# Performance work log

Measured on AMD Instinct MI355X. Metric: run time of the kernel, lower is better.

Reference implementation:

```python
import jax, jax.numpy as jnp
import numpy as np

# Grid configuration (from PointBasedTransformConfig / data dict)
G = 64                      # mast3r grid size per axis
NUM_VOXELS = G * G * G      # 262144
K = 16                      # max_points_in_voxel
RES = 0.02                  # mast3r_grid_resolution
MIN_CORNER = -(G * RES) / 2.0  # cube centered at origin, side G*RES = 1.28
N_POINTS = 2_000_000


def setup_inputs() -> dict:
    key = jax.random.key(0)
    k1, k2, k3, k4 = jax.random.split(key, 4)
    # points uniform in [-0.8, 0.8]^3 so roughly half are inside the 1.28 cube
    pts_0 = (jax.random.uniform(k1, (N_POINTS, 3), dtype=jnp.float32) - 0.5) * 1.6
    conf = jax.random.uniform(k2, (N_POINTS,), dtype=jnp.float32)
    desc = jax.random.normal(k3, (N_POINTS, 24), dtype=jnp.float32)
    desc_conf = jax.random.normal(k4, (N_POINTS,), dtype=jnp.float32)
    return {"pts_0": pts_0, "conf": conf, "desc": desc, "desc_conf": desc_conf}


def _voxelize(pts_0, conf):
    """Returns pts_in_grid: (NUM_VOXELS, K) int32 point indices (or -1)."""
    n = pts_0.shape[0]
    # voxel index per point; out-of-bounds points get sentinel id NUM_VOXELS
    idx = jnp.floor((pts_0 - MIN_CORNER) / RES).astype(jnp.int32)  # (N,3)
    valid = jnp.all((idx >= 0) & (idx < G), axis=-1)               # (N,)
    vox = idx[:, 0] * (G * G) + idx[:, 1] * G + idx[:, 2]
    vox = jnp.where(valid, vox, NUM_VOXELS)
    # stable sort by confidence, descending (jnp.argsort is stable)
    order_conf = jnp.argsort(-conf)                 # point ids, conf-desc order
    vox_c = vox[order_conf]
    # stable sort by voxel id (preserves conf-desc order within each voxel)
    order_vox = jnp.argsort(vox_c)
    vox_s = vox_c[order_vox]                        # sorted voxel ids
    pid_s = order_conf[order_vox]                   # original point ids
    # bincount + exclusive cumsum -> per-voxel offsets -> position within voxel
    counts = jnp.bincount(vox_s, length=NUM_VOXELS + 1)
    offsets = jnp.cumsum(counts) - counts
    pos = jnp.arange(n, dtype=jnp.int32) - offsets[vox_s].astype(jnp.int32)
    # capacity-bounded scatter of point ids into the voxel grid
    ok = (pos < K) & (vox_s < NUM_VOXELS)
    rows = jnp.where(ok, vox_s, NUM_VOXELS)         # dump row for rejects
    cols = jnp.where(ok, pos, 0)
    vals = jnp.where(ok, pid_s, -1).astype(jnp.int32)
    grid = jnp.full((NUM_VOXELS + 1, K), -1, dtype=jnp.int32)
    grid = grid.at[rows, cols].set(vals)
    return grid[:NUM_VOXELS]


def reference(pts_0, conf, desc, desc_conf):
    pts_in_grid = _voxelize(pts_0, conf)            # (V, K) int32
    # gather per-point features into the grid; empty slots -> 0
    feat = jnp.concatenate(
        [pts_0, conf[:, None], desc, desc_conf[:, None]], axis=-1
    )                                               # (N, 29)
    safe = jnp.maximum(pts_in_grid, 0)
    occ = (pts_in_grid >= 0)[..., None].astype(feat.dtype)
    X = feat[safe] * occ                            # (V, K, 29)
    return pts_in_grid, X
```

## Files before the change

kernel.cpp:

```cpp
#include <hip/hip_runtime.h>
#include <limits.h>
#include <math.h>

#define GRID 64
#define NUM_VOXELS (GRID * GRID * GRID)
#define KSLOTS 16
#define CAP 32
#define FEAT 29

typedef float f32x4 __attribute__((ext_vector_type(4)));

__global__ __launch_bounds__(256) void scatter_kernel(
    const float* __restrict__ pts, const float* __restrict__ conf, int n,
    int* __restrict__ cnt, unsigned long long* __restrict__ buf) {
    int i = blockIdx.x * blockDim.x + threadIdx.x;
    if (i >= n) return;
    const float minc = (float)(-(64.0 * 0.02) / 2.0);
    const float rinv = 50.0f;
    float x = pts[(size_t)i * 3 + 0];
    float y = pts[(size_t)i * 3 + 1];
    float z = pts[(size_t)i * 3 + 2];
    int ix = (int)floorf((x - minc) * rinv);
    int iy = (int)floorf((y - minc) * rinv);
    int iz = (int)floorf((z - minc) * rinv);
    if ((unsigned)ix >= GRID || (unsigned)iy >= GRID || (unsigned)iz >= GRID) return;
    int v = ix * (GRID * GRID) + iy * GRID + iz;
    int pos = atomicAdd(&cnt[v], 1);
    if (pos < CAP) {
        unsigned int cb = __float_as_uint(conf[i]);
        unsigned long long key =
            ((unsigned long long)cb << 32) | (unsigned int)(~i);
        buf[(size_t)v * CAP + pos] = key;
    }
}

__global__ __launch_bounds__(256) void select_kernel(
    const int* __restrict__ cnt, const unsigned long long* __restrict__ buf,
    float* __restrict__ out_idx, float* __restrict__ stagedC) {
    int v = blockIdx.x * blockDim.x + threadIdx.x;
    if (v >= NUM_VOXELS) return;
    unsigned long long top[KSLOTS];
    #pragma unroll
    for (int s = 0; s < KSLOTS; ++s) top[s] = 0ULL;
    int n = cnt[v];
    if (n > CAP) n = CAP;
    const unsigned long long* row = buf + (size_t)v * CAP;
    for (int j = 0; j < n; ++j) {
        unsigned long long key = row[j];
        #pragma unroll
        for (int s = 0; s < KSLOTS; ++s) {
            unsigned long long hi = key > top[s] ? key : top[s];
            unsigned long long lo = key > top[s] ? top[s] : key;
            top[s] = hi;
            key    = lo;
        }
    }
    float* o = out_idx + (size_t)v * KSLOTS;
    float* c = stagedC + (size_t)v * KSLOTS;
    #pragma unroll
    for (int s = 0; s < KSLOTS; ++s) {
        unsigned long long k = top[s];
        o[s] = (float)((k != 0ULL) ? (int)(~(unsigned int)k) : -1);
        c[s] = __uint_as_float((unsigned int)(k >> 32));
    }
}

__global__ __launch_bounds__(256) void gather_kernel(
    const float* __restrict__ pts, const float* __restrict__ stagedC,
    const float* __restrict__ desc, const float* __restrict__ desc_conf,
    const float* __restrict__ out_idx, float* __restrict__ out_feat) {
    const int t = threadIdx.x;
    const size_t slot0 = (size_t)blockIdx.x * 256;
    const size_t slot  = slot0 + t;
    __shared__ __align__(16) float st[256 * FEAT];
    int pid = (int)out_idx[slot];
    float f[FEAT];
    #pragma unroll
    for (int e = 0; e < FEAT; ++e) f[e] = 0.0f;
    if (pid >= 0) {
        f[0] = pts[(size_t)pid * 3 + 0];
        f[1] = pts[(size_t)pid * 3 + 1];
        f[2] = pts[(size_t)pid * 3 + 2];
        f[3] = stagedC[slot];
        const f32x4* d4 = (const f32x4*)(desc) + (size_t)pid * 6;
        #pragma unroll
        for (int q = 0; q < 6; ++q) {
            f32x4 d = d4[q];
            f[4 + q * 4 + 0] = d.x; f[4 + q * 4 + 1] = d.y;
            f[4 + q * 4 + 2] = d.z; f[4 + q * 4 + 3] = d.w;
        }
        f[28] = desc_conf[pid];
    }
    #pragma unroll
    for (int e = 0; e < FEAT; ++e) st[t * FEAT + e] = f[e];
    __syncthreads();
    f32x4* dst = (f32x4*)(out_feat + slot0 * FEAT);
    const f32x4* src = (const f32x4*)st;
    #pragma unroll
    for (int k = t; k < 256 * FEAT / 4; k += 256)
        __builtin_nontemporal_store(src[k], &dst[k]);
}

__global__ __launch_bounds__(256) void select_kernel_nf(
    const int* __restrict__ cnt, const unsigned long long* __restrict__ buf,
    float* __restrict__ out_idx) {
    int v = blockIdx.x * blockDim.x + threadIdx.x;
    if (v >= NUM_VOXELS) return;
    unsigned long long top[KSLOTS];
    #pragma unroll
    for (int s = 0; s < KSLOTS; ++s) top[s] = 0ULL;
    int n = cnt[v];
    if (n > CAP) n = CAP;
    const unsigned long long* row = buf + (size_t)v * CAP;
    for (int j = 0; j < n; ++j) {
        unsigned long long key = row[j];
        #pragma unroll
        for (int s = 0; s < KSLOTS; ++s) {
            unsigned long long hi = key > top[s] ? key : top[s];
            unsigned long long lo = key > top[s] ? top[s] : key;
            top[s] = hi;
            key    = lo;
        }
    }
    float* o = out_idx + (size_t)v * KSLOTS;
    #pragma unroll
    for (int s = 0; s < KSLOTS; ++s) {
        unsigned long long k = top[s];
        o[s] = (float)((k != 0ULL) ? (int)(~(unsigned int)k) : -1);
    }
}

__global__ __launch_bounds__(256) void gather_kernel_nf(
    const float* __restrict__ pts, const float* __restrict__ conf,
    const float* __restrict__ desc, const float* __restrict__ desc_conf,
    const float* __restrict__ out_idx, float* __restrict__ out_feat) {
    const int t = threadIdx.x;
    const size_t slot0 = (size_t)blockIdx.x * 256;
    const size_t slot  = slot0 + t;
    __shared__ __align__(16) float st[256 * FEAT];
    int pid = (int)out_idx[slot];
    float f[FEAT];
    #pragma unroll
    for (int e = 0; e < FEAT; ++e) f[e] = 0.0f;
    if (pid >= 0) {
        f[0] = pts[(size_t)pid * 3 + 0];
        f[1] = pts[(size_t)pid * 3 + 1];
        f[2] = pts[(size_t)pid * 3 + 2];
        f[3] = conf[pid];
        const f32x4* d4 = (const f32x4*)(desc) + (size_t)pid * 6;
        #pragma unroll
        for (int q = 0; q < 6; ++q) {
            f32x4 d = d4[q];
            f[4 + q * 4 + 0] = d.x; f[4 + q * 4 + 1] = d.y;
            f[4 + q * 4 + 2] = d.z; f[4 + q * 4 + 3] = d.w;
        }
        f[28] = desc_conf[pid];
    }
    #pragma unroll
    for (int e = 0; e < FEAT; ++e) st[t * FEAT + e] = f[e];
    __syncthreads();
    f32x4* dst = (f32x4*)(out_feat + slot0 * FEAT);
    const f32x4* src = (const f32x4*)st;
    #pragma unroll
    for (int k = t; k < 256 * FEAT / 4; k += 256)
        __builtin_nontemporal_store(src[k], &dst[k]);
}

extern "C" void kernel_launch(void* const* d_in, const int* in_sizes, int n_in,
                              void* d_out, int out_size, void* d_ws, size_t ws_size,
                              hipStream_t stream) {
    const float* pts       = (const float*)d_in[0];
    const float* conf      = (const float*)d_in[1];
    const float* desc      = (const float*)d_in[2];
    const float* desc_conf = (const float*)d_in[3];
    const int n = in_sizes[1];

    float* out_idx  = (float*)d_out;
    float* out_feat = out_idx + (size_t)NUM_VOXELS * KSLOTS;

    const size_t sz_cnt  = (size_t)NUM_VOXELS * 4;
    const size_t sz_buf  = (size_t)NUM_VOXELS * CAP * 8;
    const size_t sz_stgc = (size_t)NUM_VOXELS * KSLOTS * 4;

    if (ws_size >= sz_cnt + sz_buf + sz_stgc) {
        int* cnt = (int*)d_ws;
        unsigned long long* buf = (unsigned long long*)((char*)d_ws + sz_cnt);
        float* stagedC = (float*)((char*)d_ws + sz_cnt + sz_buf);
        (void)hipMemsetAsync(cnt, 0, sz_cnt, stream);
        scatter_kernel<<<(n + 255) / 256, 256, 0, stream>>>(pts, conf, n, cnt, buf);
        select_kernel<<<NUM_VOXELS / 256, 256, 0, stream>>>(cnt, buf, out_idx, stagedC);
        gather_kernel<<<(NUM_VOXELS * KSLOTS) / 256, 256, 0, stream>>>(
            pts, stagedC, desc, desc_conf, out_idx, out_feat);
    } else {
        int* cnt = (int*)out_feat;
        unsigned long long* buf = (unsigned long long*)(out_feat + NUM_VOXELS);
        (void)hipMemsetAsync(cnt, 0, sz_cnt, stream);
        scatter_kernel<<<(n + 255) / 256, 256, 0, stream>>>(pts, conf, n, cnt, buf);
        select_kernel_nf<<<NUM_VOXELS / 256, 256, 0, stream>>>(cnt, buf, out_idx);
        gather_kernel_nf<<<(NUM_VOXELS * KSLOTS) / 256, 256, 0, stream>>>(
            pts, conf, desc, desc_conf, out_idx, out_feat);
    }
}
```

Baseline: 226.7 us.

## Carry point coords and desc_conf in voxel buffer to cut random gathers

The scatter kernel now writes a 32-byte record per point: a sort key (conf bits, a 21-bit point id, room for the slot index) plus x, y, z and desc_conf. The select kernel recovers the payload through the slot index in the winning key and stages coordinates, conf and desc_conf contiguously per output slot. The gather kernel then only randomly fetches desc, which removes scattered pts and desc_conf reads. In exchange the scatter buffer grows fourfold (256 MB of workspace), scatter and select write more, and the fast path now requires n to fit in 21 bits.

```diff
diff --git a/kernel.cpp b/kernel.cpp
--- a/kernel.cpp
+++ b/kernel.cpp
@@ -7,12 +7,15 @@
 #define KSLOTS 16
 #define CAP 32
 #define FEAT 29
+#define PIDBITS 0x1FFFFFu
 
 typedef float f32x4 __attribute__((ext_vector_type(4)));
+typedef unsigned long long u64;
 
 __global__ __launch_bounds__(256) void scatter_kernel(
-    const float* __restrict__ pts, const float* __restrict__ conf, int n,
-    int* __restrict__ cnt, unsigned long long* __restrict__ buf) {
+    const float* __restrict__ pts, const float* __restrict__ conf,
+    const float* __restrict__ desc_conf, int n,
+    int* __restrict__ cnt, u64* __restrict__ buf) {
     int i = blockIdx.x * blockDim.x + threadIdx.x;
     if (i >= n) return;
     const float minc = (float)(-(64.0 * 0.02) / 2.0);
@@ -28,60 +31,76 @@
     int pos = atomicAdd(&cnt[v], 1);
     if (pos < CAP) {
         unsigned int cb = __float_as_uint(conf[i]);
-        unsigned long long key =
-            ((unsigned long long)cb << 32) | (unsigned int)(~i);
-        buf[(size_t)v * CAP + pos] = key;
+        unsigned int lo = ((~(unsigned)i) & PIDBITS) << 11;
+        u64* e = buf + ((size_t)v * CAP + pos) * 4;
+        e[0] = ((u64)cb << 32) | lo;
+        f32x4 pl = {x, y, z, desc_conf[i]};
+        *(f32x4*)(e + 2) = pl;
     }
 }
 
 __global__ __launch_bounds__(256) void select_kernel(
-    const int* __restrict__ cnt, const unsigned long long* __restrict__ buf,
-    float* __restrict__ out_idx, float* __restrict__ stagedC) {
+    const int* __restrict__ cnt, const u64* __restrict__ buf,
+    float* __restrict__ out_idx, f32x4* __restrict__ stagedA,
+    float* __restrict__ stagedB) {
     int v = blockIdx.x * blockDim.x + threadIdx.x;
     if (v >= NUM_VOXELS) return;
-    unsigned long long top[KSLOTS];
+    u64 top[KSLOTS];
     #pragma unroll
     for (int s = 0; s < KSLOTS; ++s) top[s] = 0ULL;
     int n = cnt[v];
     if (n > CAP) n = CAP;
-    const unsigned long long* row = buf + (size_t)v * CAP;
+    const u64* row = buf + (size_t)v * CAP * 4;
     for (int j = 0; j < n; ++j) {
-        unsigned long long key = row[j];
+        u64 key = row[(size_t)j * 4] | (unsigned)j;
         #pragma unroll
         for (int s = 0; s < KSLOTS; ++s) {
-            unsigned long long hi = key > top[s] ? key : top[s];
-            unsigned long long lo = key > top[s] ? top[s] : key;
+            u64 hi = key > top[s] ? key : top[s];
+            u64 lo = key > top[s] ? top[s] : key;
             top[s] = hi;
             key    = lo;
         }
     }
-    float* o = out_idx + (size_t)v * KSLOTS;
-    float* c = stagedC + (size_t)v * KSLOTS;
+    float* o  = out_idx + (size_t)v * KSLOTS;
+    f32x4* sa = stagedA + (size_t)v * KSLOTS;
+    float* sb = stagedB + (size_t)v * KSLOTS;
     #pragma unroll
     for (int s = 0; s < KSLOTS; ++s) {
-        unsigned long long k = top[s];
-        o[s] = (float)((k != 0ULL) ? (int)(~(unsigned int)k) : -1);
-        c[s] = __uint_as_float((unsigned int)(k >> 32));
+        u64 a = top[s];
+        float pidf = -1.0f;
+        f32x4 pl = {0.0f, 0.0f, 0.0f, 0.0f};
+        float dc = 0.0f;
+        if (a != 0ULL) {
+            int j = (int)(a & 31u);
+            f32x4 p = *(const f32x4*)(row + (size_t)j * 4 + 2);
+            int pid = (int)(PIDBITS & ~(unsigned)(a >> 11));
+            pidf = (float)pid;
+            pl.x = p.x; pl.y = p.y; pl.z = p.z;
+            pl.w = __uint_as_float((unsigned)(a >> 32));
+            dc = p.w;
+        }
+        o[s]  = pidf;
+        sa[s] = pl;
+        sb[s] = dc;
     }
 }
 
 __global__ __launch_bounds__(256) void gather_kernel(
-    const float* __restrict__ pts, const float* __restrict__ stagedC,
-    const float* __restrict__ desc, const float* __restrict__ desc_conf,
+    const f32x4* __restrict__ stagedA, const float* __restrict__ stagedB,
+    const float* __restrict__ desc,
     const float* __restrict__ out_idx, float* __restrict__ out_feat) {
     const int t = threadIdx.x;
     const size_t slot0 = (size_t)blockIdx.x * 256;
     const size_t slot  = slot0 + t;
     __shared__ __align__(16) float st[256 * FEAT];
     int pid = (int)out_idx[slot];
+    f32x4 a = stagedA[slot];
+    float dc = stagedB[slot];
     float f[FEAT];
     #pragma unroll
     for (int e = 0; e < FEAT; ++e) f[e] = 0.0f;
+    f[0] = a.x; f[1] = a.y; f[2] = a.z; f[3] = a.w; f[28] = dc;
     if (pid >= 0) {
-        f[0] = pts[(size_t)pid * 3 + 0];
-        f[1] = pts[(size_t)pid * 3 + 1];
-        f[2] = pts[(size_t)pid * 3 + 2];
-        f[3] = stagedC[slot];
         const f32x4* d4 = (const f32x4*)(desc) + (size_t)pid * 6;
         #pragma unroll
         for (int q = 0; q < 6; ++q) {
@@ -89,7 +108,6 @@
             f[4 + q * 4 + 0] = d.x; f[4 + q * 4 + 1] = d.y;
             f[4 + q * 4 + 2] = d.z; f[4 + q * 4 + 3] = d.w;
         }
-        f[28] = desc_conf[pid];
     }
     #pragma unroll
     for (int e = 0; e < FEAT; ++e) st[t * FEAT + e] = f[e];
@@ -101,23 +119,45 @@
         __builtin_nontemporal_store(src[k], &dst[k]);
 }
 
+__global__ __launch_bounds__(256) void scatter_kernel_nf(
+    const float* __restrict__ pts, const float* __restrict__ conf, int n,
+    int* __restrict__ cnt, u64* __restrict__ buf) {
+    int i = blockIdx.x * blockDim.x + threadIdx.x;
+    if (i >= n) return;
+    const float minc = (float)(-(64.0 * 0.02) / 2.0);
+    const float rinv = 50.0f;
+    float x = pts[(size_t)i * 3 + 0];
+    float y = pts[(size_t)i * 3 + 1];
+    float z = pts[(size_t)i * 3 + 2];
+    int ix = (int)floorf((x - minc) * rinv);
+    int iy = (int)floorf((y - minc) * rinv);
+    int iz = (int)floorf((z - minc) * rinv);
+    if ((unsigned)ix >= GRID || (unsigned)iy >= GRID || (unsigned)iz >= GRID) return;
+    int v = ix * (GRID * GRID) + iy * GRID + iz;
+    int pos = atomicAdd(&cnt[v], 1);
+    if (pos < CAP) {
+        unsigned int cb = __float_as_uint(conf[i]);
+        buf[(size_t)v * CAP + pos] = ((u64)cb << 32) | (unsigned int)(~i);
+    }
+}
+
 __global__ __launch_bounds__(256) void select_kernel_nf(
-    const int* __restrict__ cnt, const unsigned long long* __restrict__ buf,
+    const int* __restrict__ cnt, const u64* __restrict__ buf,
     float* __restrict__ out_idx) {
     int v = blockIdx.x * blockDim.x + threadIdx.x;
     if (v >= NUM_VOXELS) return;
-    unsigned long long top[KSLOTS];
+    u64 top[KSLOTS];
     #pragma unroll
     for (int s = 0; s < KSLOTS; ++s) top[s] = 0ULL;
     int n = cnt[v];
     if (n > CAP) n = CAP;
-    const unsigned long long* row = buf + (size_t)v * CAP;
+    const u64* row = buf + (size_t)v * CAP;
     for (int j = 0; j < n; ++j) {
-        unsigned long long key = row[j];
+        u64 key = row[j];
         #pragma unroll
         for (int s = 0; s < KSLOTS; ++s) {
-            unsigned long long hi = key > top[s] ? key : top[s];
-            unsigned long long lo = key > top[s] ? top[s] : key;
+            u64 hi = key > top[s] ? key : top[s];
+            u64 lo = key > top[s] ? top[s] : key;
             top[s] = hi;
             key    = lo;
         }
@@ -125,7 +165,7 @@
     float* o = out_idx + (size_t)v * KSLOTS;
     #pragma unroll
     for (int s = 0; s < KSLOTS; ++s) {
-        unsigned long long k = top[s];
+        u64 k = top[s];
         o[s] = (float)((k != 0ULL) ? (int)(~(unsigned int)k) : -1);
     }
 }
@@ -178,24 +218,28 @@
     float* out_idx  = (float*)d_out;
     float* out_feat = out_idx + (size_t)NUM_VOXELS * KSLOTS;
 
-    const size_t sz_cnt  = (size_t)NUM_VOXELS * 4;
-    const size_t sz_buf  = (size_t)NUM_VOXELS * CAP * 8;
-    const size_t sz_stgc = (size_t)NUM_VOXELS * KSLOTS * 4;
-
-    if (ws_size >= sz_cnt + sz_buf + sz_stgc) {
+    const size_t sz_cnt = (size_t)NUM_VOXELS * 4;
+    const size_t sz_buf = (size_t)NUM_VOXELS * CAP * 32;
+    const size_t sz_sa  = (size_t)NUM_VOXELS * KSLOTS * 16;
+    const size_t sz_sb  = (size_t)NUM_VOXELS * KSLOTS * 4;
+
+    if (ws_size >= sz_cnt + sz_buf + sz_sa + sz_sb && (unsigned)n <= PIDBITS) {
         int* cnt = (int*)d_ws;
-        unsigned long long* buf = (unsigned long long*)((char*)d_ws + sz_cnt);
-        float* stagedC = (float*)((char*)d_ws + sz_cnt + sz_buf);
+        u64* buf = (u64*)((char*)d_ws + sz_cnt);
+        f32x4* stagedA = (f32x4*)((char*)d_ws + sz_cnt + sz_buf);
+        float* stagedB = (float*)((char*)d_ws + sz_cnt + sz_buf + sz_sa);
         (void)hipMemsetAsync(cnt, 0, sz_cnt, stream);
-        scatter_kernel<<<(n + 255) / 256, 256, 0, stream>>>(pts, conf, n, cnt, buf);
-        select_kernel<<<NUM_VOXELS / 256, 256, 0, stream>>>(cnt, buf, out_idx, stagedC);
+        scatter_kernel<<<(n + 255) / 256, 256, 0, stream>>>(
+            pts, conf, desc_conf, n, cnt, buf);
+        select_kernel<<<NUM_VOXELS / 256, 256, 0, stream>>>(
+            cnt, buf, out_idx, stagedA, stagedB);
         gather_kernel<<<(NUM_VOXELS * KSLOTS) / 256, 256, 0, stream>>>(
-            pts, stagedC, desc, desc_conf, out_idx, out_feat);
+            stagedA, stagedB, desc, out_idx, out_feat);
     } else {
         int* cnt = (int*)out_feat;
-        unsigned long long* buf = (unsigned long long*)(out_feat + NUM_VOXELS);
+        u64* buf = (u64*)(out_feat + NUM_VOXELS);
         (void)hipMemsetAsync(cnt, 0, sz_cnt, stream);
-        scatter_kernel<<<(n + 255) / 256, 256, 0, stream>>>(pts, conf, n, cnt, buf);
+        scatter_kernel_nf<<<(n + 255) / 256, 256, 0, stream>>>(pts, conf, n, cnt, buf);
         select_kernel_nf<<<NUM_VOXELS / 256, 256, 0, stream>>>(cnt, buf, out_idx);
         gather_kernel_nf<<<(NUM_VOXELS * KSLOTS) / 256, 256, 0, stream>>>(
             pts, conf, desc, desc_conf, out_idx, out_feat);
```

Measured after the change: 316.7 us. 1.4x slower.
